# Optimization experiments

Measured on AMD Instinct MI355X. Metric: run time of the kernel, lower is better.

The kernel has to match this reference:

```python
import jax, jax.numpy as jnp
import numpy as np

B, L, D, H, DFF, K, NLVL = 8, 16384, 256, 8, 1024, 1000, 4
HD = D // H            # 32 head dim
NP = HD // 2           # 16 rotary pairs per head
GY, GX, GL = 6, 6, 4   # pairs allocated to y, x, level position dims
SPATIAL_THETA, LEVEL_THETA = 100.0, 10.0


def _freqs(n, theta):
    return theta ** (-jnp.arange(n, dtype=jnp.float32) / n)


def _layer_norm(x, g, b):
    mu = jnp.mean(x, axis=-1, keepdims=True)
    v = jnp.mean(jnp.square(x - mu), axis=-1, keepdims=True)
    return (x - mu) * jax.lax.rsqrt(v + 1e-5) * g + b


def _apply_rope(t, cos, sin):
    # t: [B, K, H, HD]; cos/sin: [B, K, 1, NP] (heads shared)
    tr = t.reshape(t.shape[:-1] + (NP, 2))
    t1, t2 = tr[..., 0], tr[..., 1]
    return jnp.stack([t1 * cos - t2 * sin, t1 * sin + t2 * cos], axis=-1).reshape(t.shape)


def setup_inputs() -> dict:
    key = jax.random.key(0)
    ks = jax.random.split(key, 12)
    N = B * L
    s = 0.02
    batch_idx = jnp.repeat(jnp.arange(B, dtype=jnp.int32), L)
    spat = jax.random.randint(ks[3], (2, N), 0, 32, dtype=jnp.int32)
    lvl = jax.random.randint(ks[4], (1, N), 0, NLVL, dtype=jnp.int32)
    return {
        "queries": jax.random.normal(ks[0], (N, D), jnp.float32),
        "query_batch_offsets": jnp.arange(B + 1, dtype=jnp.int32) * L,
        "token_predicted_salience_score": jax.random.uniform(ks[1], (N,), jnp.float32),
        "token_electron_scores": jax.random.uniform(ks[2], (N,), jnp.float32),
        "query_spatial_indices": jnp.concatenate([batch_idx[None], spat, lvl], axis=0),
        "stacked_feature_maps": jnp.zeros((1,), jnp.float32),  # unused (neighborhood attn off)
        "level_spatial_shapes": jnp.array([[256, 256], [128, 128], [64, 64], [32, 32]], jnp.int32),
        "Wqkv": jax.random.normal(ks[5], (D, 3 * D), jnp.float32) * s,
        "Wo": jax.random.normal(ks[6], (D, D), jnp.float32) * s,
        "ln1_g": jnp.ones((D,), jnp.float32), "ln1_b": jnp.zeros((D,), jnp.float32),
        "W1": jax.random.normal(ks[7], (D, DFF), jnp.float32) * s,
        "b1": jnp.zeros((DFF,), jnp.float32),
        "W2": jax.random.normal(ks[8], (DFF, D), jnp.float32) * s,
        "b2": jnp.zeros((D,), jnp.float32),
        "ln2_g": jnp.ones((D,), jnp.float32), "ln2_b": jnp.zeros((D,), jnp.float32),
    }


def reference(queries, query_batch_offsets, token_predicted_salience_score,
              query_spatial_indices, stacked_feature_maps, level_spatial_shapes,
              token_electron_scores, Wqkv, Wo, ln1_g, ln1_b, W1, b1, W2, b2, ln2_g, ln2_b):
    # --- per-batch top-k salience selection (equal-length fast path) ---
    scores = (token_electron_scores + token_predicted_salience_score).reshape(B, L)
    _, idx = jax.lax.top_k(jax.lax.stop_gradient(scores), K)           # [B, K]
    topk_indices = (idx + query_batch_offsets[:-1, None]).reshape(-1)  # [B*K]

    # --- gather selected tokens ---
    x = queries[topk_indices]                          # [B*K, D]
    sp = query_spatial_indices[:, topk_indices]        # [4, B*K]
    pos = sp[1:3].T.astype(jnp.float32)                # [B*K, 2] (y, x)
    lvl = sp[3]
    shapes_f = level_spatial_shapes.astype(jnp.float32)
    pos = pos * (shapes_f[0][None, :] / shapes_f[lvl])  # rescale to finest level
    lvl_f = lvl.astype(jnp.float32)

    ang = jnp.concatenate([
        pos[:, 0:1] * _freqs(GY, SPATIAL_THETA)[None, :],
        pos[:, 1:2] * _freqs(GX, SPATIAL_THETA)[None, :],
        lvl_f[:, None] * _freqs(GL, LEVEL_THETA)[None, :],
    ], axis=-1)                                        # [B*K, NP]
    cos = jnp.cos(ang).reshape(B, K, 1, NP)
    sin = jnp.sin(ang).reshape(B, K, 1, NP)

    # --- pre-norm RoPE self-attention over selected tokens ---
    h = _layer_norm(x, ln1_g, ln1_b)
    qkv = h @ Wqkv                                     # [B*K, 3D]
    q, k, v = [t.reshape(B, K, H, HD) for t in jnp.split(qkv, 3, axis=-1)]
    q = _apply_rope(q, cos, sin)
    k = _apply_rope(k, cos, sin)
    att = jnp.einsum('bqhd,bkhd->bhqk', q, k) / jnp.sqrt(jnp.float32(HD))
    att = jax.nn.softmax(att, axis=-1)
    out = jnp.einsum('bhqk,bkhd->bqhd', att, v).reshape(B * K, D) @ Wo
    sa_out = x + out

    # --- scatter (index_copy) back ---
    queries = queries.at[topk_indices].set(sa_out)

    # --- pre-norm FFN on all tokens ---
    h2 = _layer_norm(queries, ln2_g, ln2_b)
    queries = queries + (jax.nn.gelu(h2 @ W1 + b1) @ W2 + b2)
    return queries
```

## Files before the change

kernel.cpp:

```cpp
#include <hip/hip_runtime.h>
#include <hip/hip_bf16.h>
#include <math.h>

#define B_   8
#define L_   16384
#define D_   256
#define H_   8
#define DFF_ 1024
#define KSEL 1000
#define NTOK (B_*KSEL)
#define NALL (B_*L_)
#define HD_  32
#define NP_  16

typedef float f32x4 __attribute__((ext_vector_type(4)));
typedef short s16x8 __attribute__((ext_vector_type(8)));
typedef unsigned short u16x8 __attribute__((ext_vector_type(8)));
typedef unsigned short u16x4 __attribute__((ext_vector_type(4)));

static __device__ __forceinline__ unsigned short f2bf(float f) {
  __bf16 b = (__bf16)f;
  return __builtin_bit_cast(unsigned short, b);
}
static __device__ __forceinline__ float bf2f(unsigned short h) {
  return __uint_as_float(((unsigned)h) << 16);
}
static __device__ __forceinline__ f32x4 mfma_bf16(s16x8 a, s16x8 b, f32x4 c) {
  return __builtin_amdgcn_mfma_f32_16x16x32_bf16(a, b, c, 0, 0, 0);
}

__global__ __launch_bounds__(256) void transpose_all(
    const float* Wqkv, const float* Wo, const float* W1, const float* W2,
    unsigned short* Wqkvt, unsigned short* Wot, unsigned short* W1t, unsigned short* W2t) {
  __shared__ float tile[32][33];
  int bid = blockIdx.x;
  const float* src; unsigned short* dst; int K, N, tl;
  if (bid < 192)      { src = Wqkv; dst = Wqkvt; K = 256;  N = 768;  tl = bid; }
  else if (bid < 256) { src = Wo;   dst = Wot;   K = 256;  N = 256;  tl = bid - 192; }
  else if (bid < 512) { src = W1;   dst = W1t;   K = 256;  N = 1024; tl = bid - 256; }
  else                { src = W2;   dst = W2t;   K = 1024; N = 256;  tl = bid - 512; }
  int ntx = N >> 5;
  int n0 = (tl % ntx) * 32, k0 = (tl / ntx) * 32;
  int tx = threadIdx.x & 31, ty = threadIdx.x >> 5;
#pragma unroll
  for (int r = 0; r < 32; r += 8)
    tile[ty + r][tx] = src[(size_t)(k0 + ty + r) * N + n0 + tx];
  __syncthreads();
#pragma unroll
  for (int r = 0; r < 32; r += 8)
    dst[(size_t)(n0 + ty + r) * K + k0 + tx] = f2bf(tile[tx][ty + r]);
}

__global__ __launch_bounds__(1024) void topk_kernel(const float* es, const float* ss, int* out_idx) {
  __shared__ int wsum[16];
  __shared__ int chunk_base;
  int b = blockIdx.x;
  int t = threadIdx.x;
  int lane = t & 63, w = t >> 6;
  int base = b * L_;
  unsigned kreg[16];
#pragma unroll
  for (int ci = 0; ci < 16; ++ci) {
    int i = ci * 1024 + t;
    float f = es[base + i] + ss[base + i];
    unsigned u = __float_as_uint(f);
    kreg[ci] = (u & 0x80000000u) ? ~u : (u | 0x80000000u);
  }
  unsigned v = 0;
  for (int bit = 31; bit >= 0; --bit) {
    unsigned cand = v | (1u << bit);
    int c = 0;
#pragma unroll
    for (int ci = 0; ci < 16; ++ci) c += (kreg[ci] >= cand) ? 1 : 0;
    for (int m = 1; m < 64; m <<= 1) c += __shfl_xor(c, m);
    if (lane == 0) wsum[w] = c;
    __syncthreads();
    int tot = 0;
#pragma unroll
    for (int j = 0; j < 16; ++j) tot += wsum[j];
    if (tot >= KSEL) v = cand;
    __syncthreads();
  }
  if (t == 0) chunk_base = 0;
  __syncthreads();
  for (int pass = 0; pass < 2; ++pass) {
    for (int ci = 0; ci < 16; ++ci) {
      bool pred = (pass == 0) ? (kreg[ci] > v) : (kreg[ci] == v);
      unsigned long long mask = __ballot(pred);
      if (lane == 0) wsum[w] = __popcll(mask);
      __syncthreads();
      int wbase = chunk_base;
      for (int j = 0; j < w; ++j) wbase += wsum[j];
      if (pred) {
        int pos = wbase + __popcll(mask & ((1ull << lane) - 1ull));
        if (pos < KSEL) out_idx[b * KSEL + pos] = base + ci * 1024 + t;
      }
      __syncthreads();
      if (t == 0) { int tt = 0; for (int j = 0; j < 16; ++j) tt += wsum[j]; chunk_base += tt; }
      __syncthreads();
    }
  }
}

__global__ __launch_bounds__(256) void gather_ln_rope(
    const float* queries, const int* idx, const int* spat, const int* shapes,
    const float* g1, const float* b1ln, unsigned short* h, float* cosb, float* sinb) {
  int tok = blockIdx.x;
  int t = threadIdx.x;
  int gidx = idx[tok];
  float x = queries[(size_t)gidx * D_ + t];
  float s1 = x, s2 = x * x;
  for (int m = 1; m < 64; m <<= 1) { s1 += __shfl_xor(s1, m); s2 += __shfl_xor(s2, m); }
  __shared__ float p1[4], p2[4];
  int w = t >> 6;
  if ((t & 63) == 0) { p1[w] = s1; p2[w] = s2; }
  __syncthreads();
  float tot  = p1[0] + p1[1] + p1[2] + p1[3];
  float tot2 = p2[0] + p2[1] + p2[2] + p2[3];
  float mu = tot / D_;
  float var = tot2 / D_ - mu * mu;
  float rs = 1.0f / sqrtf(var + 1e-5f);
  h[(size_t)tok * D_ + t] = f2bf((x - mu) * rs * g1[t] + b1ln[t]);
  if (t < NP_) {
    int yy = spat[1*(size_t)NALL + gidx];
    int xx = spat[2*(size_t)NALL + gidx];
    int lv = spat[3*(size_t)NALL + gidx];
    float ang;
    if (t < 6) {
      float sc = (float)shapes[0] / (float)shapes[lv*2+0];
      ang = (float)yy * sc * powf(100.0f, -(float)t / 6.0f);
    } else if (t < 12) {
      float sc = (float)shapes[1] / (float)shapes[lv*2+1];
      ang = (float)xx * sc * powf(100.0f, -(float)(t-6) / 6.0f);
    } else {
      ang = (float)lv * powf(10.0f, -(float)(t-12) / 4.0f);
    }
    cosb[tok*NP_ + t] = cosf(ang);
    sinb[tok*NP_ + t] = sinf(ang);
  }
}

__global__ __launch_bounds__(256) void qkv_gemm(
    const unsigned short* h, const unsigned short* Wt,
    unsigned short* qh, unsigned short* kh, unsigned short* vh) {
  __shared__ unsigned short a_lds[64][264];
  int m0 = blockIdx.y * 64;
  int n0 = blockIdx.x * 128;
  int t = threadIdx.x, lane = t & 63, w = t >> 6;
  int lm = lane & 15, lg = lane >> 4;
  for (int it = 0; it < 8; ++it) {
    int c = it*256 + t;
    int row = c >> 5, off = (c & 31) * 8;
    *(uint4*)&a_lds[row][off] = *(const uint4*)&h[(size_t)(m0+row)*D_ + off];
  }
  __syncthreads();
  f32x4 acc[8];
#pragma unroll
  for (int i = 0; i < 8; ++i) acc[i] = (f32x4){0.f,0.f,0.f,0.f};
#pragma unroll
  for (int ks = 0; ks < 8; ++ks) {
    s16x8 a = *(const s16x8*)&a_lds[w*16 + lm][ks*32 + lg*8];
#pragma unroll
    for (int nt = 0; nt < 8; ++nt) {
      s16x8 bb = *(const s16x8*)&Wt[(size_t)(n0 + nt*16 + lm)*D_ + ks*32 + lg*8];
      acc[nt] = mfma_bf16(a, bb, acc[nt]);
    }
  }
#pragma unroll
  for (int i = 0; i < 4; ++i) {
    int row = w*16 + lg*4 + i;
    int tok = m0 + row;
    int b = tok / 1000, tk = tok - b*1000;
#pragma unroll
    for (int nt = 0; nt < 8; ++nt) {
      int col = n0 + nt*16 + lm;
      int part = col >> 8;
      int within = col & 255;
      int head = within >> 5, d = within & 31;
      unsigned short* dst = part == 0 ? qh : (part == 1 ? kh : vh);
      dst[(size_t)((b*H_ + head)*1000 + tk)*HD_ + d] = f2bf(acc[nt][i]);
    }
  }
}

__global__ __launch_bounds__(256) void attn_kernel(
    const unsigned short* qh, const unsigned short* kh, const unsigned short* vh,
    const float* cosb, const float* sinb, unsigned short* obuf) {
  __shared__ unsigned short k_lds[64][40];
  __shared__ unsigned short vt_lds[32][72];
  __shared__ unsigned short p_lds[4][16][72];
  int bh = blockIdx.y;
  int b = bh >> 3, hh = bh & 7;
  int q0 = blockIdx.x * 64;
  int t = threadIdx.x, lane = t & 63, w = t >> 6;
  int lm = lane & 15, lg = lane >> 4;

  int qrow = q0 + w*16 + lm;
  int qtk = qrow < 999 ? qrow : 999;
  int qtokg = b*1000 + qtk;
  s16x8 qf;
  {
    u16x8 raw = *(const u16x8*)&qh[(size_t)(bh*1000 + qtk)*HD_ + lg*8];
    f32x4 c4 = *(const f32x4*)&cosb[(size_t)qtokg*NP_ + lg*4];
    f32x4 s4 = *(const f32x4*)&sinb[(size_t)qtokg*NP_ + lg*4];
#pragma unroll
    for (int m = 0; m < 4; ++m) {
      float t1 = bf2f(raw[2*m]), t2 = bf2f(raw[2*m+1]);
      float e = t1*c4[m] - t2*s4[m];
      float o = t1*s4[m] + t2*c4[m];
      qf[2*m]   = (short)f2bf(e);
      qf[2*m+1] = (short)f2bf(o);
    }
  }

  float m_run[4], l_run[4];
  f32x4 o_acc[2];
#pragma unroll
  for (int i = 0; i < 4; ++i) { m_run[i] = -1e30f; l_run[i] = 0.f; }
  o_acc[0] = (f32x4){0.f,0.f,0.f,0.f};
  o_acc[1] = (f32x4){0.f,0.f,0.f,0.f};

  for (int ch = 0; ch < 16; ++ch) {
    int c0 = ch * 64;
    __syncthreads();
    for (int it = 0; it < 4; ++it) {
      int pi = it*256 + t;
      int key = pi >> 4, pp = pi & 15;
      int tk = c0 + key; tk = tk < 999 ? tk : 999;
      int tokg = b*1000 + tk;
      unsigned raw = *(const unsigned*)&kh[(size_t)(bh*1000 + tk)*HD_ + pp*2];
      float cc = cosb[(size_t)tokg*NP_ + pp], scn = sinb[(size_t)tokg*NP_ + pp];
      float t1 = bf2f((unsigned short)(raw & 0xFFFFu));
      float t2 = bf2f((unsigned short)(raw >> 16));
      float e = t1*cc - t2*scn, od = t1*scn + t2*cc;
      unsigned outp = (unsigned)f2bf(e) | ((unsigned)f2bf(od) << 16);
      *(unsigned*)&k_lds[key][pp*2] = outp;
    }
    for (int it = 0; it < 4; ++it) {
      int e2 = it*256 + t;
      int key = e2 >> 4, dp = e2 & 15;
      int tk = c0 + key; tk = tk < 999 ? tk : 999;
      unsigned raw = *(const unsigned*)&vh[(size_t)(bh*1000 + tk)*HD_ + dp*2];
      vt_lds[dp*2][key]   = (unsigned short)(raw & 0xFFFFu);
      vt_lds[dp*2+1][key] = (unsigned short)(raw >> 16);
    }
    __syncthreads();
    f32x4 sacc[4];
#pragma unroll
    for (int nt = 0; nt < 4; ++nt) {
      sacc[nt] = (f32x4){0.f,0.f,0.f,0.f};
      s16x8 bb = *(const s16x8*)&k_lds[nt*16 + lm][lg*8];
      sacc[nt] = mfma_bf16(qf, bb, sacc[nt]);
    }
    const float scale = 0.17677669529663687f;
#pragma unroll
    for (int nt = 0; nt < 4; ++nt) {
      int col = c0 + nt*16 + lm;
      bool valid = col < 1000;
#pragma unroll
      for (int i = 0; i < 4; ++i) sacc[nt][i] = valid ? sacc[nt][i]*scale : -1e30f;
    }
#pragma unroll
    for (int i = 0; i < 4; ++i) {
      float mx = fmaxf(fmaxf(sacc[0][i], sacc[1][i]), fmaxf(sacc[2][i], sacc[3][i]));
      for (int m = 1; m < 16; m <<= 1) mx = fmaxf(mx, __shfl_xor(mx, m));
      float mn = fmaxf(m_run[i], mx);
      float alpha = __expf(m_run[i] - mn);
      float rsum = 0.f;
#pragma unroll
      for (int nt = 0; nt < 4; ++nt) { float p = __expf(sacc[nt][i] - mn); sacc[nt][i] = p; rsum += p; }
      for (int m = 1; m < 16; m <<= 1) rsum += __shfl_xor(rsum, m);
      l_run[i] = l_run[i]*alpha + rsum;
      m_run[i] = mn;
      o_acc[0][i] *= alpha; o_acc[1][i] *= alpha;
    }
#pragma unroll
    for (int nt = 0; nt < 4; ++nt)
#pragma unroll
      for (int i = 0; i < 4; ++i)
        p_lds[w][lg*4 + i][nt*16 + lm] = f2bf(sacc[nt][i]);
#pragma unroll
    for (int kk = 0; kk < 2; ++kk) {
      s16x8 pf = *(const s16x8*)&p_lds[w][lm][kk*32 + lg*8];
#pragma unroll
      for (int dt = 0; dt < 2; ++dt) {
        s16x8 vf = *(const s16x8*)&vt_lds[dt*16 + lm][kk*32 + lg*8];
        o_acc[dt] = mfma_bf16(pf, vf, o_acc[dt]);
      }
    }
  }
#pragma unroll
  for (int i = 0; i < 4; ++i) {
    int qr = q0 + w*16 + lg*4 + i;
    if (qr < 1000) {
      float innorm = 1.0f / l_run[i];
      int tokg = b*1000 + qr;
#pragma unroll
      for (int dt = 0; dt < 2; ++dt)
        obuf[(size_t)tokg*D_ + hh*HD_ + dt*16 + lm] = f2bf(o_acc[dt][i] * innorm);
    }
  }
}

__global__ __launch_bounds__(256) void wo_scatter(
    const unsigned short* obuf, const unsigned short* Wot,
    const float* queries, const int* idx, float* sa, int* slot_of) {
  __shared__ unsigned short a_lds[64][264];
  int m0 = blockIdx.x * 64;
  int t = threadIdx.x, lane = t & 63, w = t >> 6;
  int lm = lane & 15, lg = lane >> 4;
  for (int it = 0; it < 8; ++it) {
    int c = it*256 + t;
    int row = c >> 5, off = (c & 31) * 8;
    *(uint4*)&a_lds[row][off] = *(const uint4*)&obuf[(size_t)(m0+row)*D_ + off];
  }
  if (t < 64) { int tok = m0 + t; slot_of[idx[tok]] = tok; }
  __syncthreads();
  f32x4 acc[16];
#pragma unroll
  for (int i = 0; i < 16; ++i) acc[i] = (f32x4){0.f,0.f,0.f,0.f};
#pragma unroll
  for (int ks = 0; ks < 8; ++ks) {
    s16x8 a = *(const s16x8*)&a_lds[w*16 + lm][ks*32 + lg*8];
#pragma unroll
    for (int nt = 0; nt < 16; ++nt) {
      s16x8 bb = *(const s16x8*)&Wot[(size_t)(nt*16 + lm)*D_ + ks*32 + lg*8];
      acc[nt] = mfma_bf16(a, bb, acc[nt]);
    }
  }
#pragma unroll
  for (int i = 0; i < 4; ++i) {
    int row = w*16 + lg*4 + i;
    int tok = m0 + row;
    int g = idx[tok];
#pragma unroll
    for (int nt = 0; nt < 16; ++nt) {
      int col = nt*16 + lm;
      sa[(size_t)tok*D_ + col] = queries[(size_t)g*D_ + col] + acc[nt][i];
    }
  }
}

__global__ __launch_bounds__(512, 4) void ffn_kernel(
    const float* queries, const float* sa, const int* slot_of,
    const unsigned short* W1t, const unsigned short* W2t,
    const float* b1, const float* b2, const float* g2, const float* bb2,
    float* out) {
  __shared__ unsigned short h2[64][264];
  __shared__ unsigned short c1[64][264];
  int m0 = blockIdx.x * 64;
  int t = threadIdx.x, lane = t & 63, w = t >> 6;
  int lm = lane & 15, lg = lane >> 4;
  {
    f32x4 g2v  = *(const f32x4*)&g2[lane*4];
    f32x4 bb2v = *(const f32x4*)&bb2[lane*4];
#pragma unroll
    for (int rr = 0; rr < 8; ++rr) {
      int row = w*8 + rr;
      int grow = m0 + row;
      int slot = slot_of[grow];
      const float* xb = (slot >= 0) ? (sa + (size_t)slot * D_) : (queries + (size_t)grow * D_);
      f32x4 x = *(const f32x4*)&xb[lane*4];
      float s1 = x[0]+x[1]+x[2]+x[3];
      float s2 = x[0]*x[0]+x[1]*x[1]+x[2]*x[2]+x[3]*x[3];
      for (int m = 1; m < 64; m <<= 1) { s1 += __shfl_xor(s1, m); s2 += __shfl_xor(s2, m); }
      float mu = s1 * (1.0f/D_);
      float rs = __builtin_amdgcn_rsqf(s2 * (1.0f/D_) - mu*mu + 1e-5f);
      u16x4 hv;
#pragma unroll
      for (int j = 0; j < 4; ++j) hv[j] = f2bf((x[j]-mu)*rs*g2v[j] + bb2v[j]);
      *(u16x4*)&h2[row][lane*4] = hv;
    }
  }
  __syncthreads();

  f32x4 acc2[2][4];
#pragma unroll
  for (int at = 0; at < 2; ++at)
#pragma unroll
    for (int rt = 0; rt < 4; ++rt) acc2[at][rt] = (f32x4){0.f,0.f,0.f,0.f};

  const unsigned short* w2p = W2t + (size_t)(w*32 + lm) * DFF_ + lg*8;

  for (int chn = 0; chn < 4; ++chn) {
    int d0 = chn * 256;
    f32x4 acc1[2][4];
#pragma unroll
    for (int at = 0; at < 2; ++at)
#pragma unroll
      for (int rt = 0; rt < 4; ++rt) acc1[at][rt] = (f32x4){0.f,0.f,0.f,0.f};
    const unsigned short* w1p = W1t + (size_t)(d0 + w*32 + lm) * D_ + lg*8;
#pragma unroll
    for (int ks = 0; ks < 8; ++ks) {
      s16x8 wa0 = *(const s16x8*)(w1p + ks*32);
      s16x8 wa1 = *(const s16x8*)(w1p + 16*D_ + ks*32);
      s16x8 f0 = *(const s16x8*)&h2[lm     ][ks*32 + lg*8];
      s16x8 f1 = *(const s16x8*)&h2[lm + 16][ks*32 + lg*8];
      s16x8 f2 = *(const s16x8*)&h2[lm + 32][ks*32 + lg*8];
      s16x8 f3 = *(const s16x8*)&h2[lm + 48][ks*32 + lg*8];
      acc1[0][0] = mfma_bf16(wa0, f0, acc1[0][0]);
      acc1[0][1] = mfma_bf16(wa0, f1, acc1[0][1]);
      acc1[0][2] = mfma_bf16(wa0, f2, acc1[0][2]);
      acc1[0][3] = mfma_bf16(wa0, f3, acc1[0][3]);
      acc1[1][0] = mfma_bf16(wa1, f0, acc1[1][0]);
      acc1[1][1] = mfma_bf16(wa1, f1, acc1[1][1]);
      acc1[1][2] = mfma_bf16(wa1, f2, acc1[1][2]);
      acc1[1][3] = mfma_bf16(wa1, f3, acc1[1][3]);
    }
#pragma unroll
    for (int at = 0; at < 2; ++at) {
      f32x4 b1v = *(const f32x4*)&b1[d0 + w*32 + at*16 + lg*4];
#pragma unroll
      for (int rt = 0; rt < 4; ++rt) {
        u16x4 pv;
#pragma unroll
        for (int i = 0; i < 4; ++i) {
          float xv = acc1[at][rt][i] + b1v[i];
          float z = 0.7978845608028654f * xv * fmaf(xv*xv, 0.044715f, 1.0f);
          float e = __builtin_amdgcn_exp2f(z * -2.885390081777927f);
          float rcp = __builtin_amdgcn_rcpf(1.0f + e);
          float th = fmaf(-2.0f*e, rcp, 1.0f);
          float y = 0.5f * xv;
          y = fmaf(y, th, y);
          pv[i] = f2bf(y);
        }
        *(u16x4*)&c1[rt*16 + lm][w*32 + at*16 + lg*4] = pv;
      }
    }
    __syncthreads();
#pragma unroll
    for (int ks = 0; ks < 8; ++ks) {
      s16x8 wa0 = *(const s16x8*)(w2p + d0 + ks*32);
      s16x8 wa1 = *(const s16x8*)(w2p + (size_t)16*DFF_ + d0 + ks*32);
      s16x8 f0 = *(const s16x8*)&c1[lm     ][ks*32 + lg*8];
      s16x8 f1 = *(const s16x8*)&c1[lm + 16][ks*32 + lg*8];
      s16x8 f2 = *(const s16x8*)&c1[lm + 32][ks*32 + lg*8];
      s16x8 f3 = *(const s16x8*)&c1[lm + 48][ks*32 + lg*8];
      acc2[0][0] = mfma_bf16(wa0, f0, acc2[0][0]);
      acc2[0][1] = mfma_bf16(wa0, f1, acc2[0][1]);
      acc2[0][2] = mfma_bf16(wa0, f2, acc2[0][2]);
      acc2[0][3] = mfma_bf16(wa0, f3, acc2[0][3]);
      acc2[1][0] = mfma_bf16(wa1, f0, acc2[1][0]);
      acc2[1][1] = mfma_bf16(wa1, f1, acc2[1][1]);
      acc2[1][2] = mfma_bf16(wa1, f2, acc2[1][2]);
      acc2[1][3] = mfma_bf16(wa1, f3, acc2[1][3]);
    }
    __syncthreads();
  }
#pragma unroll
  for (int rt = 0; rt < 4; ++rt) {
    int grow = m0 + rt*16 + lm;
    int slot = slot_of[grow];
    const float* xb = (slot >= 0) ? (sa + (size_t)slot * D_) : (queries + (size_t)grow * D_);
#pragma unroll
    for (int at = 0; at < 2; ++at) {
      int oc = w*32 + at*16 + lg*4;
      f32x4 b2v = *(const f32x4*)&b2[oc];
      f32x4 xv = *(const f32x4*)&xb[oc];
      f32x4 v;
#pragma unroll
      for (int i = 0; i < 4; ++i) v[i] = acc2[at][rt][i] + xv[i] + b2v[i];
      *(f32x4*)&out[(size_t)grow * D_ + oc] = v;
    }
  }
}

extern "C" void kernel_launch(void* const* d_in, const int* in_sizes, int n_in,
                              void* d_out, int out_size, void* d_ws, size_t ws_size,
                              hipStream_t stream) {
  const float* queries = (const float*)d_in[0];
  const float* sal   = (const float*)d_in[2];
  const float* ele   = (const float*)d_in[3];
  const int*   spat  = (const int*)d_in[4];
  const int*   shapes= (const int*)d_in[6];
  const float* Wqkv  = (const float*)d_in[7];
  const float* Wo    = (const float*)d_in[8];
  const float* ln1g  = (const float*)d_in[9];
  const float* ln1b  = (const float*)d_in[10];
  const float* W1    = (const float*)d_in[11];
  const float* b1    = (const float*)d_in[12];
  const float* W2    = (const float*)d_in[13];
  const float* b2    = (const float*)d_in[14];
  const float* ln2g  = (const float*)d_in[15];
  const float* ln2b  = (const float*)d_in[16];
  float* out = (float*)d_out;

  char* ws = (char*)d_ws;
  size_t off = 0;
  auto alloc = [&](size_t bytes) -> void* {
    void* p = ws + off;
    off = (off + bytes + 255) & ~(size_t)255;
    return p;
  };
  int*            idxb  = (int*)alloc((size_t)NTOK * 4);
  unsigned short* h     = (unsigned short*)alloc((size_t)NTOK * D_ * 2);
  float*          cosb  = (float*)alloc((size_t)NTOK * NP_ * 4);
  float*          sinb  = (float*)alloc((size_t)NTOK * NP_ * 4);
  unsigned short* qh    = (unsigned short*)alloc((size_t)NTOK * D_ * 2);
  unsigned short* kh    = (unsigned short*)alloc((size_t)NTOK * D_ * 2);
  unsigned short* vh    = (unsigned short*)alloc((size_t)NTOK * D_ * 2);
  unsigned short* obuf  = (unsigned short*)alloc((size_t)NTOK * D_ * 2);
  unsigned short* Wqkvt = (unsigned short*)alloc((size_t)768 * 256 * 2);
  unsigned short* Wot   = (unsigned short*)alloc((size_t)256 * 256 * 2);
  unsigned short* W1t   = (unsigned short*)alloc((size_t)1024 * 256 * 2);
  unsigned short* W2t   = (unsigned short*)alloc((size_t)256 * 1024 * 2);
  float*          sa    = (float*)alloc((size_t)NTOK * D_ * 4);
  int*            slot  = (int*)alloc((size_t)NALL * 4);

  hipMemsetAsync(slot, 0xFF, (size_t)NALL * 4, stream);
  transpose_all<<<768, 256, 0, stream>>>(Wqkv, Wo, W1, W2, Wqkvt, Wot, W1t, W2t);
  topk_kernel<<<B_, 1024, 0, stream>>>(ele, sal, idxb);
  gather_ln_rope<<<NTOK, 256, 0, stream>>>(queries, idxb, spat, shapes, ln1g, ln1b, h, cosb, sinb);
  qkv_gemm<<<dim3(6, 125), 256, 0, stream>>>(h, Wqkvt, qh, kh, vh);
  attn_kernel<<<dim3(16, 64), 256, 0, stream>>>(qh, kh, vh, cosb, sinb, obuf);
  wo_scatter<<<125, 256, 0, stream>>>(obuf, Wot, queries, idxb, sa, slot);
  ffn_kernel<<<2048, 512, 0, stream>>>(queries, sa, slot, W1t, W2t, b1, b2, ln2g, ln2b, out);
}
```

Baseline: 495.4 us.

## Double-buffer FFN hidden chunks with XOR-swizzled shared memory layout

Restructures the fused FFN kernel to process the hidden dimension in eight 128-wide chunks with a double-buffered c1 tile. Each iteration computes GEMM1+GELU for the next chunk while running GEMM2 on the current one, which halves the barriers per chunk pair. The padded shared arrays are replaced with XOR-swizzled layouts to avoid LDS bank conflicts without padding. The trade-off is smaller per-wave GEMM1 tiles (16 columns instead of 32), which means less reuse of the h2 fragment loads per weight load.

```diff
diff --git a/kernel.cpp b/kernel.cpp
--- a/kernel.cpp
+++ b/kernel.cpp
@@ -346,11 +346,13 @@
     const unsigned short* W1t, const unsigned short* W2t,
     const float* b1, const float* b2, const float* g2, const float* bb2,
     float* out) {
-  __shared__ unsigned short h2[64][264];
-  __shared__ unsigned short c1[64][264];
+  __shared__ unsigned short h2[64*256];
+  __shared__ unsigned short c1[2*64*128];
   int m0 = blockIdx.x * 64;
   int t = threadIdx.x, lane = t & 63, w = t >> 6;
   int lm = lane & 15, lg = lane >> 4;
+  int x4 = (lm & 7) << 4;
+
   {
     f32x4 g2v  = *(const f32x4*)&g2[lane*4];
     f32x4 bb2v = *(const f32x4*)&bb2[lane*4];
@@ -369,10 +371,9 @@
       u16x4 hv;
 #pragma unroll
       for (int j = 0; j < 4; ++j) hv[j] = f2bf((x[j]-mu)*rs*g2v[j] + bb2v[j]);
-      *(u16x4*)&h2[row][lane*4] = hv;
-    }
-  }
-  __syncthreads();
+      *(u16x4*)((char*)h2 + row*512 + ((lane*8) ^ ((row & 7) << 4))) = hv;
+    }
+  }
 
   f32x4 acc2[2][4];
 #pragma unroll
@@ -380,73 +381,68 @@
 #pragma unroll
     for (int rt = 0; rt < 4; ++rt) acc2[at][rt] = (f32x4){0.f,0.f,0.f,0.f};
 
-  const unsigned short* w2p = W2t + (size_t)(w*32 + lm) * DFF_ + lg*8;
-
-  for (int chn = 0; chn < 4; ++chn) {
-    int d0 = chn * 256;
-    f32x4 acc1[2][4];
-#pragma unroll
-    for (int at = 0; at < 2; ++at)
-#pragma unroll
-      for (int rt = 0; rt < 4; ++rt) acc1[at][rt] = (f32x4){0.f,0.f,0.f,0.f};
-    const unsigned short* w1p = W1t + (size_t)(d0 + w*32 + lm) * D_ + lg*8;
+  const char* h2c = (const char*)h2;
+  char* c1base = (char*)c1;
+  const unsigned short* w1base = W1t + (size_t)(w*16 + lm) * D_ + lg*8;
+  const unsigned short* w2base = W2t + (size_t)(w*32 + lm) * DFF_ + lg*8;
+
+  auto run_g1 = [&](int hc, int buf) {
+    f32x4 acc1[4];
+#pragma unroll
+    for (int rt = 0; rt < 4; ++rt) acc1[rt] = (f32x4){0.f,0.f,0.f,0.f};
+    const unsigned short* w1p = w1base + (size_t)hc * 128 * D_;
 #pragma unroll
     for (int ks = 0; ks < 8; ++ks) {
-      s16x8 wa0 = *(const s16x8*)(w1p + ks*32);
-      s16x8 wa1 = *(const s16x8*)(w1p + 16*D_ + ks*32);
-      s16x8 f0 = *(const s16x8*)&h2[lm     ][ks*32 + lg*8];
-      s16x8 f1 = *(const s16x8*)&h2[lm + 16][ks*32 + lg*8];
-      s16x8 f2 = *(const s16x8*)&h2[lm + 32][ks*32 + lg*8];
-      s16x8 f3 = *(const s16x8*)&h2[lm + 48][ks*32 + lg*8];
-      acc1[0][0] = mfma_bf16(wa0, f0, acc1[0][0]);
-      acc1[0][1] = mfma_bf16(wa0, f1, acc1[0][1]);
-      acc1[0][2] = mfma_bf16(wa0, f2, acc1[0][2]);
-      acc1[0][3] = mfma_bf16(wa0, f3, acc1[0][3]);
-      acc1[1][0] = mfma_bf16(wa1, f0, acc1[1][0]);
-      acc1[1][1] = mfma_bf16(wa1, f1, acc1[1][1]);
-      acc1[1][2] = mfma_bf16(wa1, f2, acc1[1][2]);
-      acc1[1][3] = mfma_bf16(wa1, f3, acc1[1][3]);
-    }
-#pragma unroll
-    for (int at = 0; at < 2; ++at) {
-      f32x4 b1v = *(const f32x4*)&b1[d0 + w*32 + at*16 + lg*4];
+      s16x8 wa = *(const s16x8*)(w1p + ks*32);
 #pragma unroll
       for (int rt = 0; rt < 4; ++rt) {
-        u16x4 pv;
-#pragma unroll
-        for (int i = 0; i < 4; ++i) {
-          float xv = acc1[at][rt][i] + b1v[i];
-          float z = 0.7978845608028654f * xv * fmaf(xv*xv, 0.044715f, 1.0f);
-          float e = __builtin_amdgcn_exp2f(z * -2.885390081777927f);
-          float rcp = __builtin_amdgcn_rcpf(1.0f + e);
-          float th = fmaf(-2.0f*e, rcp, 1.0f);
-          float y = 0.5f * xv;
-          y = fmaf(y, th, y);
-          pv[i] = f2bf(y);
-        }
-        *(u16x4*)&c1[rt*16 + lm][w*32 + at*16 + lg*4] = pv;
+        s16x8 f = *(const s16x8*)(h2c + (rt*16 + lm)*512 + ((ks*64 + lg*16) ^ x4));
+        acc1[rt] = mfma_bf16(wa, f, acc1[rt]);
       }
     }
+    f32x4 b1v = *(const f32x4*)&b1[hc*128 + w*16 + lg*4];
+    char* cb = c1base + buf * 16384;
+#pragma unroll
+    for (int rt = 0; rt < 4; ++rt) {
+      u16x4 pv;
+#pragma unroll
+      for (int i = 0; i < 4; ++i) {
+        float xv = acc1[rt][i] + b1v[i];
+        float z = 0.7978845608028654f * xv * fmaf(xv*xv, 0.044715f, 1.0f);
+        float e = __builtin_amdgcn_exp2f(z * -2.885390081777927f);
+        float rcp = __builtin_amdgcn_rcpf(1.0f + e);
+        float th = fmaf(-2.0f*e, rcp, 1.0f);
+        float y = 0.5f * xv;
+        y = fmaf(y, th, y);
+        pv[i] = f2bf(y);
+      }
+      *(u16x4*)(cb + (rt*16 + lm)*256 + ((w*32 + lg*8) ^ x4)) = pv;
+    }
+  };
+  auto run_g2 = [&](int hc, int buf) {
+    const char* cb = c1base + buf * 16384;
+#pragma unroll
+    for (int ks = 0; ks < 4; ++ks) {
+      s16x8 wa0 = *(const s16x8*)(w2base + hc*128 + ks*32);
+      s16x8 wa1 = *(const s16x8*)(w2base + (size_t)16*DFF_ + hc*128 + ks*32);
+#pragma unroll
+      for (int rt = 0; rt < 4; ++rt) {
+        s16x8 f = *(const s16x8*)(cb + (rt*16 + lm)*256 + ((ks*64 + lg*16) ^ x4));
+        acc2[0][rt] = mfma_bf16(wa0, f, acc2[0][rt]);
+        acc2[1][rt] = mfma_bf16(wa1, f, acc2[1][rt]);
+      }
+    }
+  };
+
+  __syncthreads();
+  run_g1(0, 0);
+  __syncthreads();
+  for (int hc = 0; hc < 8; ++hc) {
+    if (hc < 7) run_g1(hc + 1, (hc + 1) & 1);
+    run_g2(hc, hc & 1);
     __syncthreads();
-#pragma unroll
-    for (int ks = 0; ks < 8; ++ks) {
-      s16x8 wa0 = *(const s16x8*)(w2p + d0 + ks*32);
-      s16x8 wa1 = *(const s16x8*)(w2p + (size_t)16*DFF_ + d0 + ks*32);
-      s16x8 f0 = *(const s16x8*)&c1[lm     ][ks*32 + lg*8];
-      s16x8 f1 = *(const s16x8*)&c1[lm + 16][ks*32 + lg*8];
-      s16x8 f2 = *(const s16x8*)&c1[lm + 32][ks*32 + lg*8];
-      s16x8 f3 = *(const s16x8*)&c1[lm + 48][ks*32 + lg*8];
-      acc2[0][0] = mfma_bf16(wa0, f0, acc2[0][0]);
-      acc2[0][1] = mfma_bf16(wa0, f1, acc2[0][1]);
-      acc2[0][2] = mfma_bf16(wa0, f2, acc2[0][2]);
-      acc2[0][3] = mfma_bf16(wa0, f3, acc2[0][3]);
-      acc2[1][0] = mfma_bf16(wa1, f0, acc2[1][0]);
-      acc2[1][1] = mfma_bf16(wa1, f1, acc2[1][1]);
-      acc2[1][2] = mfma_bf16(wa1, f2, acc2[1][2]);
-      acc2[1][3] = mfma_bf16(wa1, f3, acc2[1][3]);
-    }
-    __syncthreads();
-  }
+  }
+
 #pragma unroll
   for (int rt = 0; rt < 4; ++rt) {
     int grow = m0 + rt*16 + lm;
@@ -507,7 +503,7 @@
   float*          sa    = (float*)alloc((size_t)NTOK * D_ * 4);
   int*            slot  = (int*)alloc((size_t)NALL * 4);
 
-  hipMemsetAsync(slot, 0xFF, (size_t)NALL * 4, stream);
+  (void)hipMemsetAsync(slot, 0xFF, (size_t)NALL * 4, stream);
   transpose_all<<<768, 256, 0, stream>>>(Wqkv, Wo, W1, W2, Wqkvt, Wot, W1t, W2t);
   topk_kernel<<<B_, 1024, 0, stream>>>(ele, sal, idxb);
   gather_ln_rope<<<NTOK, 256, 0, stream>>>(queries, idxb, spat, shapes, ln1g, ln1b, h, cosb, sinb);
```

New measurement: 491.0 us. No clear change (-0.9%).
